# Kernel optimization log

Hardware: AMD Instinct MI355X
Metric: run time of the kernel (lower is better)

Reference implementation:

```python
import jax, jax.numpy as jnp
import numpy as np

B, T, K, DIM = 32, 12, 16, 512
H0, H1 = 512, 256


def setup_inputs() -> dict:
    key = jax.random.key(0)
    k0, k1, k2, k3, k4 = jax.random.split(key, 5)
    return {
        "sets_of_objects": jax.random.normal(k0, (B, T, K, DIM), dtype=jnp.float32),
        "W0": jax.random.normal(k1, (2 * DIM, H0), dtype=jnp.float32) * 0.02,
        "b0": jnp.zeros((H0,), dtype=jnp.float32),
        "W1": jax.random.normal(k2, (H0, H1), dtype=jnp.float32) * 0.02,
        "b1": jnp.zeros((H1,), dtype=jnp.float32),
        "D": DIM,
    }


def reference(sets_of_objects, W0, b0, W1, b1, D):
    Bb, Tt, Kk, Dm = sets_of_objects.shape
    Tm1 = Tt - 1
    # Eval path: for each t in 1..T-1, original code builds all-pairs concat of
    # O_t with itself (O_1 is unused in create_inter_object_cat), runs the MLP,
    # then avg-pools over t identical copies (no-op on e) and clamps the summed mask.
    O_t = sets_of_objects[:, 1:]                                   # [B, T-1, K, D]
    A = jnp.broadcast_to(O_t[:, :, :, None, :], (Bb, Tm1, Kk, Kk, Dm))   # first obj k repeated
    Bo = jnp.broadcast_to(O_t[:, :, None, :, :], (Bb, Tm1, Kk, Kk, Dm))  # second obj j
    pairs = jnp.concatenate([A, Bo], axis=-1).reshape(Bb, Tm1, Kk * Kk, 2 * Dm)
    # EncoderMLP: Linear -> ReLU per hidden layer
    h = jax.nn.relu(pairs @ W0 + b0)                               # [B, T-1, K*K, H0]
    e = jax.nn.relu(h @ W1 + b1)                                   # [B, T-1, K*K, H1]
    # object-presence masks (clamp of feature sums)
    is_first = jnp.clip(pairs[..., :D].sum(-1), 0.0, 1.0)          # [B, T-1, K*K]
    is_second = jnp.clip(pairs[..., D:].sum(-1), 0.0, 1.0)
    # clamp(sum over t identical copies, 0, 1) == clamp(t * v, 0, 1)
    counts = jnp.arange(1, Tt, dtype=e.dtype)[None, :, None]
    is_obj = jnp.clip(counts * is_first * is_second, 0.0, 1.0)
    return e, is_obj
```

## Files before the change

kernel.cpp:

```cpp
#include <hip/hip_runtime.h>
#include <hip/hip_bf16.h>

#define B_    32
#define T_    12
#define TM1   11
#define K_    16
#define DIM_  512
#define H0_   512
#define H1_   256
#define NROWS 5632
#define NBT   352
#define E_ELEMS (NBT*256*H1_)

typedef __bf16 bf16x8 __attribute__((ext_vector_type(8)));
typedef float  f32x16 __attribute__((ext_vector_type(16)));
typedef float  f32x4  __attribute__((ext_vector_type(4)));
typedef float  f32x2  __attribute__((ext_vector_type(2)));
typedef unsigned u32x4 __attribute__((ext_vector_type(4)));

#define OFRAG_OFF   0
#define W0FRAG_OFF  5767168
#define W1FRAG_OFF  (W0FRAG_OFF + 1048576)
#define UB_OFF      (W1FRAG_OFF + 262144)
#define VSW_OFF     (UB_OFF + 5767168)

__device__ __forceinline__ unsigned bf_rn(float f) {
    unsigned u = __float_as_uint(f);
    return (u + 0x7fffu + ((u >> 16) & 1u)) >> 16;
}
__device__ __forceinline__ unsigned pk_bf16(float lo, float hi) {
    return bf_rn(lo) | (bf_rn(hi) << 16);
}
__device__ __forceinline__ unsigned short f2bf(float f) {
    return (unsigned short)bf_rn(f);
}
__device__ __forceinline__ float bfu_lo(unsigned u) { return __uint_as_float(u << 16); }
__device__ __forceinline__ float bfu_hi(unsigned u) { return __uint_as_float(u & 0xffff0000u); }
__device__ __forceinline__ void gl2lds16(const char* g, char* l) {
    __builtin_amdgcn_global_load_lds(
        (const __attribute__((address_space(1))) unsigned*)(const void*)g,
        (__attribute__((address_space(3))) unsigned*)(void*)l, 16, 0, 0);
}

__global__ __launch_bounds__(256) void k_prep(const float* __restrict__ W0,
                                              const float* __restrict__ W1,
                                              const float* __restrict__ O,
                                              char* __restrict__ ws)
{
    const int unit = blockIdx.x * 4 + (threadIdx.x >> 6);
    const int l = threadIdx.x & 63;
    if (unit < 1280) {
        const float* src; size_t dstoff; int stride;
        if (unit < 1024) {
            int half = unit >> 9, s = (unit >> 4) & 31, nt = unit & 15;
            int k = s*16 + (l >> 5)*8;
            int n = nt*32 + (l & 31);
            src = W0 + (size_t)(half*512 + k) * H0_ + n;
            stride = H0_;
            dstoff = W0FRAG_OFF + (((size_t)(half*32 + s)*16 + nt)*64 + l)*16;
        } else {
            int r = unit - 1024; int s = r >> 3, ct = r & 7;
            int k = s*16 + (l >> 5)*8;
            int n = ct*32 + (l & 31);
            src = W1 + (size_t)k * H1_ + n;
            stride = H1_;
            dstoff = W1FRAG_OFF + (((size_t)(s*8 + ct))*64 + l)*16;
        }
        float f[8];
        #pragma unroll
        for (int j = 0; j < 8; ++j) f[j] = src[(size_t)j * stride];
        u32x4 o = { pk_bf16(f[0],f[1]), pk_bf16(f[2],f[3]), pk_bf16(f[4],f[5]), pk_bf16(f[6],f[7]) };
        *(u32x4*)(ws + dstoff) = o;
    } else {
        const int u = unit - 1280;
        const int s = u / 176, mt = u % 176;
        const int row = mt*32 + (l & 31);
        const int b  = row / (TM1*K_);
        const int rem = row % (TM1*K_);
        const int t  = rem / K_;
        const int i  = rem % K_;
        const float* src = O + (((size_t)(b*T_ + t + 1)*K_ + i)*DIM_) + s*16 + (l >> 5)*8;
        float4 a = *(const float4*)src;
        float4 c = *(const float4*)(src + 4);
        u32x4 o = { pk_bf16(a.x,a.y), pk_bf16(a.z,a.w), pk_bf16(c.x,c.y), pk_bf16(c.z,c.w) };
        *(u32x4*)(ws + OFRAG_OFF + ((size_t)(s*176 + mt)*64 + l)*16) = o;
    }
}

__global__ __launch_bounds__(256) void k_uv(char* __restrict__ ws,
                                            const float* __restrict__ b0)
{
    const int mb = blockIdx.x;
    const int t  = threadIdx.x, l = t & 63;
    const int nb = blockIdx.y * 4 + (t >> 6);
    const int half = nb >> 3;
    const char* Ag = ws + OFRAG_OFF + ((size_t)(mb*2)*64 + l)*16;
    const char* Bg = ws + W0FRAG_OFF + (size_t)half*524288 + ((size_t)((nb&7)*2)*64 + l)*16;
    const size_t AS = 176*1024, BS = 16*1024;

    f32x16 acc[2][2];
    #pragma unroll
    for (int p = 0; p < 2; ++p)
        #pragma unroll
        for (int c = 0; c < 2; ++c)
            #pragma unroll
            for (int r = 0; r < 16; ++r) acc[p][c][r] = 0.f;

    u32x4 aA[2], bA[2], aB[2], bB[2];
    #pragma unroll
    for (int p = 0; p < 2; ++p) {
        aA[p] = *(const u32x4*)(Ag + 0*AS + p*1024);
        bA[p] = *(const u32x4*)(Bg + 0*BS + p*1024);
        aB[p] = *(const u32x4*)(Ag + 1*AS + p*1024);
        bB[p] = *(const u32x4*)(Bg + 1*BS + p*1024);
    }

    for (int ss = 0; ss < 32; ss += 2) {
        {
            union { u32x4 u[2]; bf16x8 b[2]; } af, bf;
            af.u[0]=aA[0]; af.u[1]=aA[1]; bf.u[0]=bA[0]; bf.u[1]=bA[1];
            if (ss + 2 < 32) {
                #pragma unroll
                for (int p = 0; p < 2; ++p) {
                    aA[p] = *(const u32x4*)(Ag + (size_t)(ss+2)*AS + p*1024);
                    bA[p] = *(const u32x4*)(Bg + (size_t)(ss+2)*BS + p*1024);
                }
            }
            acc[0][0] = __builtin_amdgcn_mfma_f32_32x32x16_bf16(af.b[0], bf.b[0], acc[0][0], 0,0,0);
            acc[0][1] = __builtin_amdgcn_mfma_f32_32x32x16_bf16(af.b[0], bf.b[1], acc[0][1], 0,0,0);
            acc[1][0] = __builtin_amdgcn_mfma_f32_32x32x16_bf16(af.b[1], bf.b[0], acc[1][0], 0,0,0);
            acc[1][1] = __builtin_amdgcn_mfma_f32_32x32x16_bf16(af.b[1], bf.b[1], acc[1][1], 0,0,0);
        }
        {
            union { u32x4 u[2]; bf16x8 b[2]; } af, bf;
            af.u[0]=aB[0]; af.u[1]=aB[1]; bf.u[0]=bB[0]; bf.u[1]=bB[1];
            if (ss + 3 < 32) {
                #pragma unroll
                for (int p = 0; p < 2; ++p) {
                    aB[p] = *(const u32x4*)(Ag + (size_t)(ss+3)*AS + p*1024);
                    bB[p] = *(const u32x4*)(Bg + (size_t)(ss+3)*BS + p*1024);
                }
            }
            acc[0][0] = __builtin_amdgcn_mfma_f32_32x32x16_bf16(af.b[0], bf.b[0], acc[0][0], 0,0,0);
            acc[0][1] = __builtin_amdgcn_mfma_f32_32x32x16_bf16(af.b[0], bf.b[1], acc[0][1], 0,0,0);
            acc[1][0] = __builtin_amdgcn_mfma_f32_32x32x16_bf16(af.b[1], bf.b[0], acc[1][0], 0,0,0);
            acc[1][1] = __builtin_amdgcn_mfma_f32_32x32x16_bf16(af.b[1], bf.b[1], acc[1][1], 0,0,0);
        }
    }

    #pragma unroll
    for (int p = 0; p < 2; ++p) {
        #pragma unroll
        for (int c = 0; c < 2; ++c) {
            const int col = (nb & 7)*64 + c*32 + (l & 31);
            const float bias = (half == 0) ? b0[col] : 0.f;
            #pragma unroll
            for (int r = 0; r < 16; ++r) {
                const int row = (r & 3) + 8*(r >> 2) + 4*(l >> 5);
                const int M = mb*64 + p*32 + row;
                const float v = acc[p][c][r] + bias;
                if (half == 0) {
                    *(unsigned short*)(ws + UB_OFF + ((size_t)M*512 + col)*2) = f2bf(v);
                } else {
                    const int bt = M >> 4, j = M & 15;
                    const int cc = col >> 3;
                    const int c2 = ((cc ^ (j & 7)) << 3) | (col & 7);
                    *(unsigned short*)(ws + VSW_OFF + ((size_t)(bt*16 + j)*512 + c2)*2) = f2bf(v);
                }
            }
        }
    }
}

__global__ __launch_bounds__(256) void k_obj(const float* __restrict__ O,
                                             float* __restrict__ out)
{
    __shared__ float red[16][16];
    __shared__ float fl[16];
    const int bt = blockIdx.x;
    const int b_ = bt / TM1, tt = bt % TM1;
    const int t  = threadIdx.x;
    const int i  = t >> 4, s = t & 15;
    const float* base = O + (((size_t)(b_ * T_ + tt + 1) * K_ + i) * DIM_) + s * 32;
    float sum = 0.f;
    #pragma unroll
    for (int q = 0; q < 8; ++q) {
        float4 v = *(const float4*)(base + q * 4);
        sum += v.x + v.y + v.z + v.w;
    }
    red[i][s] = sum;
    __syncthreads();
    if (t < 16) {
        float f = 0.f;
        #pragma unroll
        for (int s2 = 0; s2 < 16; ++s2) f += red[t][s2];
        fl[t] = fminf(fmaxf(f, 0.f), 1.f);
    }
    __syncthreads();
    const float val = fminf((float)(tt + 1) * fl[t >> 4] * fl[t & 15], 1.f);
    __builtin_nontemporal_store(val, out + (size_t)E_ELEMS + (size_t)bt * 256 + t);
}

#define WSTAGE(C, BUFOFF)                                                      \
    do {                                                                       \
        gl2lds16(Wsrc + (size_t)((C)*2 + 0)*8192, Wbuf + (BUFOFF) + wq*1024);  \
        gl2lds16(Wsrc + (size_t)((C)*2 + 1)*8192, Wbuf + (BUFOFF) + 4096 + wq*1024); \
    } while (0)

#define KSTEP_L(S, BUFOFF, ST)                                                 \
    do {                                                                       \
        const int vch_ = (((S)*2 + kc) ^ jlow_);                               \
        u32x4 vu_ = *(const u32x4*)(VsL + vch_*16);                            \
        u32x4 uu_ = *(const u32x4*)(UsL + (S)*32);                             \
        bf16x8 af_;                                                            \
        _Pragma("unroll")                                                      \
        for (int q_ = 0; q_ < 4; ++q_) {                                       \
            f32x2 u2_ = { bfu_lo(uu_[q_]), bfu_hi(uu_[q_]) };                  \
            f32x2 v2_ = { bfu_lo(vu_[q_]), bfu_hi(vu_[q_]) };                  \
            f32x2 s2_ = u2_ + v2_;                                             \
            af_[2*q_]   = (__bf16)fmaxf(s2_.x, 0.f);                           \
            af_[2*q_+1] = (__bf16)fmaxf(s2_.y, 0.f);                           \
        }                                                                      \
        union { u32x4 u[4]; bf16x8 b[4]; } wu_;                                \
        _Pragma("unroll")                                                      \
        for (int c_ = 0; c_ < 4; ++c_)                                         \
            wu_.u[c_] = *(const u32x4*)(WlL + (BUFOFF) + (ST)*4096 + c_*1024); \
        acc0 = __builtin_amdgcn_mfma_f32_32x32x16_bf16(af_, wu_.b[0], acc0, 0,0,0); \
        acc1 = __builtin_amdgcn_mfma_f32_32x32x16_bf16(af_, wu_.b[1], acc1, 0,0,0); \
        acc2 = __builtin_amdgcn_mfma_f32_32x32x16_bf16(af_, wu_.b[2], acc2, 0,0,0); \
        acc3 = __builtin_amdgcn_mfma_f32_32x32x16_bf16(af_, wu_.b[3], acc3, 0,0,0); \
    } while (0)

__global__ __launch_bounds__(256, 3) void k_e(const char* __restrict__ ws,
                                              const float* __restrict__ b1,
                                              float* __restrict__ out)
{
    __shared__ alignas(16) char lds[40960];
    char* Us   = lds;
    char* Vs   = lds + 8192;
    char* Wbuf = lds + 24576;

    const int bid = blockIdx.x;
    const int ch = bid & 1, ph = (bid >> 1) & 1, bt = bid >> 2;
    const int t = threadIdx.x, l = t & 63, wq = t >> 6;

    const char* Ug = ws + UB_OFF  + (size_t)(bt*16 + ph*8) * 1024;
    const char* Vg = ws + VSW_OFF + (size_t)bt * 16384;
    const char* Wsrc = ws + W1FRAG_OFF + (size_t)ch*4096 + (size_t)wq*1024 + (size_t)l*16;

    #pragma unroll
    for (int r = 0; r < 2; ++r) { int c = t + r*256; *(u32x4*)(Us + c*16) = *(const u32x4*)(Ug + c*16); }
    #pragma unroll
    for (int r = 0; r < 4; ++r) { int c = t + r*256; *(u32x4*)(Vs + c*16) = *(const u32x4*)(Vg + c*16); }

    WSTAGE(0, 0);
    __syncthreads();

    f32x16 acc0, acc1, acc2, acc3;
    #pragma unroll
    for (int r = 0; r < 16; ++r) { acc0[r] = 0.f; acc1[r] = 0.f; acc2[r] = 0.f; acc3[r] = 0.f; }

    const int jj    = l & 15;
    const int jlow_ = jj & 7;
    const int kc    = l >> 5;
    const int il    = wq*2 + ((l >> 4) & 1);
    const char* UsL = Us + il*1024 + kc*16;
    const char* VsL = Vs + jj*1024;
    const char* WlL = Wbuf + (size_t)l*16;

    for (int j = 0; j < 8; ++j) {
        const int c0 = j*2;
        if (c0 + 1 < 16) WSTAGE(c0+1, 8192);
        KSTEP_L(c0*2+0, 0, 0);
        KSTEP_L(c0*2+1, 0, 1);
        __syncthreads();
        if (c0 + 2 < 16) WSTAGE(c0+2, 0);
        KSTEP_L(c0*2+2, 8192, 0);
        KSTEP_L(c0*2+3, 8192, 1);
        __syncthreads();
    }

    const int colb = ch*128 + (l & 31);
    const int pr0  = ph*128 + wq*32 + 4*(l >> 5);
    float* ob = out + ((size_t)bt*256 + pr0)*256 + colb;
    #define EPI(ACC, CT)                                                       \
        do {                                                                   \
            const float bb_ = b1[colb + (CT)*32];                              \
            _Pragma("unroll")                                                  \
            for (int r_ = 0; r_ < 16; ++r_) {                                  \
                const int rr_ = (r_ & 3) + 8*(r_ >> 2);                        \
                __builtin_nontemporal_store(fmaxf(ACC[r_] + bb_, 0.f),         \
                    ob + (size_t)rr_*256 + (CT)*32);                           \
            }                                                                  \
        } while (0)
    EPI(acc0, 0);
    EPI(acc1, 1);
    EPI(acc2, 2);
    EPI(acc3, 3);
    #undef EPI
}

extern "C" void kernel_launch(void* const* d_in, const int* in_sizes, int n_in,
                              void* d_out, int out_size, void* d_ws, size_t ws_size,
                              hipStream_t stream) {
    const float* O  = (const float*)d_in[0];
    const float* W0 = (const float*)d_in[1];
    const float* b0 = (const float*)d_in[2];
    const float* W1 = (const float*)d_in[3];
    const float* b1 = (const float*)d_in[4];
    float* out = (float*)d_out;
    char* ws = (char*)d_ws;

    k_prep<<<1728, 256, 0, stream>>>(W0, W1, O, ws);
    dim3 guv(88, 4);
    k_uv<<<guv, 256, 0, stream>>>(ws, b0);
    k_obj<<<NBT, 256, 0, stream>>>(O, out);
    k_e<<<NBT * 4, 256, 0, stream>>>(ws, b1, out);
}
```

Baseline: 65.25 us.

## Make k_e blocks process two tiles, overlapping next-tile staging with epilogue

The e-kernel grid is halved from 1408 to 704 blocks, and each block now computes two output tiles back to back. The U/V/W loads for the second tile are issued before the first tile's epilogue stores, so the load latency overlaps the store phase. Block-to-tile mapping is remapped with an XCD-aware (bid&7) swizzle, and the k_obj launch is moved before k_uv. The cost is fewer resident blocks, so there may be less latency hiding across waves, and tail imbalance if 704 blocks don't fill the CUs evenly.

```diff
diff --git a/kernel.cpp b/kernel.cpp
--- a/kernel.cpp
+++ b/kernel.cpp
@@ -201,10 +201,10 @@
     __builtin_nontemporal_store(val, out + (size_t)E_ELEMS + (size_t)bt * 256 + t);
 }
 
-#define WSTAGE(C, BUFOFF)                                                      \
-    do {                                                                       \
-        gl2lds16(Wsrc + (size_t)((C)*2 + 0)*8192, Wbuf + (BUFOFF) + wq*1024);  \
-        gl2lds16(Wsrc + (size_t)((C)*2 + 1)*8192, Wbuf + (BUFOFF) + 4096 + wq*1024); \
+#define WSTAGE(C, BUFOFF, WS)                                                  \
+    do {                                                                       \
+        gl2lds16((WS) + (size_t)((C)*2 + 0)*8192, Wbuf + (BUFOFF) + wq*1024);  \
+        gl2lds16((WS) + (size_t)((C)*2 + 1)*8192, Wbuf + (BUFOFF) + 4096 + wq*1024); \
     } while (0)
 
 #define KSTEP_L(S, BUFOFF, ST)                                                 \
@@ -229,6 +229,60 @@
         acc1 = __builtin_amdgcn_mfma_f32_32x32x16_bf16(af_, wu_.b[1], acc1, 0,0,0); \
         acc2 = __builtin_amdgcn_mfma_f32_32x32x16_bf16(af_, wu_.b[2], acc2, 0,0,0); \
         acc3 = __builtin_amdgcn_mfma_f32_32x32x16_bf16(af_, wu_.b[3], acc3, 0,0,0); \
+    } while (0)
+
+#define STAGE_UV(UG, VG)                                                       \
+    do {                                                                       \
+        _Pragma("unroll")                                                      \
+        for (int r2_ = 0; r2_ < 2; ++r2_) {                                    \
+            int c_ = t + r2_*256;                                              \
+            *(u32x4*)(Us + c_*16) = *(const u32x4*)((UG) + c_*16);             \
+        }                                                                      \
+        _Pragma("unroll")                                                      \
+        for (int r2_ = 0; r2_ < 4; ++r2_) {                                    \
+            int c_ = t + r2_*256;                                              \
+            *(u32x4*)(Vs + c_*16) = *(const u32x4*)((VG) + c_*16);             \
+        }                                                                      \
+    } while (0)
+
+#define JLOOP(WS)                                                              \
+    do {                                                                       \
+        for (int j_ = 0; j_ < 8; ++j_) {                                       \
+            const int c0_ = j_*2;                                              \
+            if (c0_ + 1 < 16) WSTAGE(c0_+1, 8192, WS);                         \
+            KSTEP_L(c0_*2+0, 0, 0);                                            \
+            KSTEP_L(c0_*2+1, 0, 1);                                            \
+            __syncthreads();                                                   \
+            if (c0_ + 2 < 16) WSTAGE(c0_+2, 0, WS);                            \
+            KSTEP_L(c0_*2+2, 8192, 0);                                         \
+            KSTEP_L(c0_*2+3, 8192, 1);                                         \
+            __syncthreads();                                                   \
+        }                                                                      \
+    } while (0)
+
+#define EPILOG(BT, PH, CH)                                                     \
+    do {                                                                       \
+        const int colb_ = (CH)*128 + (l & 31);                                 \
+        const int pr0_  = (PH)*128 + wq*32 + 4*(l >> 5);                       \
+        float* ob_ = out + ((size_t)(BT)*256 + pr0_)*256 + colb_;              \
+        const float b0_ = b1[colb_ +  0], b1v_ = b1[colb_ + 32];               \
+        const float b2_ = b1[colb_ + 64], b3_  = b1[colb_ + 96];               \
+        _Pragma("unroll")                                                      \
+        for (int r_ = 0; r_ < 16; ++r_) {                                      \
+            const int rr_ = (r_ & 3) + 8*(r_ >> 2);                            \
+            __builtin_nontemporal_store(fmaxf(acc0[r_] + b0_, 0.f),  ob_ + (size_t)rr_*256 +  0); \
+            __builtin_nontemporal_store(fmaxf(acc1[r_] + b1v_, 0.f), ob_ + (size_t)rr_*256 + 32); \
+            __builtin_nontemporal_store(fmaxf(acc2[r_] + b2_, 0.f),  ob_ + (size_t)rr_*256 + 64); \
+            __builtin_nontemporal_store(fmaxf(acc3[r_] + b3_, 0.f),  ob_ + (size_t)rr_*256 + 96); \
+        }                                                                      \
+    } while (0)
+
+#define ACCINIT                                                                \
+    do {                                                                       \
+        _Pragma("unroll")                                                      \
+        for (int r2_ = 0; r2_ < 16; ++r2_) {                                   \
+            acc0[r2_] = 0.f; acc1[r2_] = 0.f; acc2[r2_] = 0.f; acc3[r2_] = 0.f;\
+        }                                                                      \
     } while (0)
 
 __global__ __launch_bounds__(256, 3) void k_e(const char* __restrict__ ws,
@@ -240,25 +294,9 @@
     char* Vs   = lds + 8192;
     char* Wbuf = lds + 24576;
 
-    const int bid = blockIdx.x;
-    const int ch = bid & 1, ph = (bid >> 1) & 1, bt = bid >> 2;
+    const int bid0 = blockIdx.x;
+    const int lane8 = bid0 & 7;
     const int t = threadIdx.x, l = t & 63, wq = t >> 6;
-
-    const char* Ug = ws + UB_OFF  + (size_t)(bt*16 + ph*8) * 1024;
-    const char* Vg = ws + VSW_OFF + (size_t)bt * 16384;
-    const char* Wsrc = ws + W1FRAG_OFF + (size_t)ch*4096 + (size_t)wq*1024 + (size_t)l*16;
-
-    #pragma unroll
-    for (int r = 0; r < 2; ++r) { int c = t + r*256; *(u32x4*)(Us + c*16) = *(const u32x4*)(Ug + c*16); }
-    #pragma unroll
-    for (int r = 0; r < 4; ++r) { int c = t + r*256; *(u32x4*)(Vs + c*16) = *(const u32x4*)(Vg + c*16); }
-
-    WSTAGE(0, 0);
-    __syncthreads();
-
-    f32x16 acc0, acc1, acc2, acc3;
-    #pragma unroll
-    for (int r = 0; r < 16; ++r) { acc0[r] = 0.f; acc1[r] = 0.f; acc2[r] = 0.f; acc3[r] = 0.f; }
 
     const int jj    = l & 15;
     const int jlow_ = jj & 7;
@@ -268,36 +306,41 @@
     const char* VsL = Vs + jj*1024;
     const char* WlL = Wbuf + (size_t)l*16;
 
-    for (int j = 0; j < 8; ++j) {
-        const int c0 = j*2;
-        if (c0 + 1 < 16) WSTAGE(c0+1, 8192);
-        KSTEP_L(c0*2+0, 0, 0);
-        KSTEP_L(c0*2+1, 0, 1);
-        __syncthreads();
-        if (c0 + 2 < 16) WSTAGE(c0+2, 0);
-        KSTEP_L(c0*2+2, 8192, 0);
-        KSTEP_L(c0*2+3, 8192, 1);
-        __syncthreads();
-    }
-
-    const int colb = ch*128 + (l & 31);
-    const int pr0  = ph*128 + wq*32 + 4*(l >> 5);
-    float* ob = out + ((size_t)bt*256 + pr0)*256 + colb;
-    #define EPI(ACC, CT)                                                       \
-        do {                                                                   \
-            const float bb_ = b1[colb + (CT)*32];                              \
-            _Pragma("unroll")                                                  \
-            for (int r_ = 0; r_ < 16; ++r_) {                                  \
-                const int rr_ = (r_ & 3) + 8*(r_ >> 2);                        \
-                __builtin_nontemporal_store(fmaxf(ACC[r_] + bb_, 0.f),         \
-                    ob + (size_t)rr_*256 + (CT)*32);                           \
-            }                                                                  \
-        } while (0)
-    EPI(acc0, 0);
-    EPI(acc1, 1);
-    EPI(acc2, 2);
-    EPI(acc3, 3);
-    #undef EPI
+    const int gA = bid0 >> 3;
+    const int qA = gA >> 4, rA = gA & 15;
+    const int btA = qA*32 + lane8*4 + (rA >> 2);
+    const int subA = rA & 3;
+    const int chA = subA & 1, phA = subA >> 1;
+    const char* UgA = ws + UB_OFF  + (size_t)(btA*16 + phA*8) * 1024;
+    const char* VgA = ws + VSW_OFF + (size_t)btA * 16384;
+    const char* WsA = ws + W1FRAG_OFF + (size_t)chA*4096 + (size_t)wq*1024 + (size_t)l*16;
+
+    const int bidB = bid0 + 704;
+    const int gB = bidB >> 3;
+    const int qB = gB >> 4, rB = gB & 15;
+    const int btB = qB*32 + lane8*4 + (rB >> 2);
+    const int subB = rB & 3;
+    const int chB = subB & 1, phB = subB >> 1;
+    const char* UgB = ws + UB_OFF  + (size_t)(btB*16 + phB*8) * 1024;
+    const char* VgB = ws + VSW_OFF + (size_t)btB * 16384;
+    const char* WsB = ws + W1FRAG_OFF + (size_t)chB*4096 + (size_t)wq*1024 + (size_t)l*16;
+
+    f32x16 acc0, acc1, acc2, acc3;
+
+    STAGE_UV(UgA, VgA);
+    WSTAGE(0, 0, WsA);
+    __syncthreads();
+    ACCINIT;
+    JLOOP(WsA);
+
+    STAGE_UV(UgB, VgB);
+    WSTAGE(0, 0, WsB);
+    EPILOG(btA, phA, chA);
+    __syncthreads();
+
+    ACCINIT;
+    JLOOP(WsB);
+    EPILOG(btB, phB, chB);
 }
 
 extern "C" void kernel_launch(void* const* d_in, const int* in_sizes, int n_in,
@@ -312,8 +355,8 @@
     char* ws = (char*)d_ws;
 
     k_prep<<<1728, 256, 0, stream>>>(W0, W1, O, ws);
+    k_obj<<<NBT, 256, 0, stream>>>(O, out);
     dim3 guv(88, 4);
     k_uv<<<guv, 256, 0, stream>>>(ws, b0);
-    k_obj<<<NBT, 256, 0, stream>>>(O, out);
-    k_e<<<NBT * 4, 256, 0, stream>>>(ws, b1, out);
-}
+    k_e<<<704, 256, 0, stream>>>(ws, b1, out);
+}
```

New measurement: 65.39 us. No clear change (+0.2%).
